# Performance work log

Hardware: AMD Instinct MI355X
Metric: run time of the kernel (lower is better)

The kernel has to match this reference:

```python
import jax, jax.numpy as jnp
import numpy as np

BN_EPS = 1e-5


def cond_conv(x, att_w, att_b, weight, pad):
    """CondConv: per-sample expert-mixed conv.
    x: [N,C,H,W]; att_w: [K,C]; att_b: [K]; weight: [K,O,I,kh,kw]; pad: (ph,pw)."""
    pooled = x.mean(axis=(2, 3))                         # [N,C]  (AdaptiveAvgPool2d(1))
    att = jax.nn.sigmoid(pooled @ att_w.T + att_b)       # [N,K]  (1x1 conv + sigmoid)
    agg_w = jnp.einsum('nk,koihw->noihw', att, weight)   # per-sample kernels [N,O,I,kh,kw]

    def conv1(xi, wi):
        return jax.lax.conv_general_dilated(
            xi[None], wi, window_strides=(1, 1),
            padding=[(pad[0], pad[0]), (pad[1], pad[1])],
            dimension_numbers=('NCHW', 'OIHW', 'NCHW'))[0]

    return jax.vmap(conv1)(x, agg_w)                     # [N,O,H,W]


def batchnorm(x, gamma, beta):
    # training-mode BN: biased batch stats over (N,H,W)
    mean = x.mean(axis=(0, 2, 3), keepdims=True)
    var = x.var(axis=(0, 2, 3), keepdims=True)
    xn = (x - mean) * jax.lax.rsqrt(var + BN_EPS)
    return xn * gamma[None, :, None, None] + beta[None, :, None, None]


def channel_shuffle(x, g):
    N, C, H, W = x.shape
    return x.reshape(N, g, C // g, H, W).transpose(0, 2, 1, 3, 4).reshape(N, C, H, W)


def setup_inputs() -> dict:
    key = jax.random.key(0)
    ks = jax.random.split(key, 8)
    N, C, H, W = 32, 256, 64, 64
    Cb, K = C // 4, 4
    inp = {
        'x': jax.random.normal(ks[0], (N, C, H, W), jnp.float32),
        'sq_att_w': jax.random.normal(ks[1], (K, Cb), jnp.float32) * 0.1,
        'sq_att_b': jnp.zeros((K,), jnp.float32),
        'sq_w': jax.random.normal(ks[2], (K, Cb, Cb, 3, 3), jnp.float32) * 0.05,
        'sq_g': jnp.ones((Cb,), jnp.float32),
        'sq_b': jnp.zeros((Cb,), jnp.float32),
        'ver_att_w': jax.random.normal(ks[3], (K, Cb), jnp.float32) * 0.1,
        'ver_att_b': jnp.zeros((K,), jnp.float32),
        'ver_w': jax.random.normal(ks[4], (K, Cb, Cb, 3, 1), jnp.float32) * 0.05,
        'ver_g': jnp.ones((Cb,), jnp.float32),
        'ver_b': jnp.zeros((Cb,), jnp.float32),
        'hor_att_w': jax.random.normal(ks[5], (K, Cb), jnp.float32) * 0.1,
        'hor_att_b': jnp.zeros((K,), jnp.float32),
        'hor_w': jax.random.normal(ks[6], (K, Cb, Cb, 1, 3), jnp.float32) * 0.05,
        'hor_g': jnp.ones((Cb,), jnp.float32),
        'hor_b': jnp.zeros((Cb,), jnp.float32),
    }
    return inp


def reference(x, sq_att_w, sq_att_b, sq_w, sq_g, sq_b,
              ver_att_w, ver_att_b, ver_w, ver_g, ver_b,
              hor_att_w, hor_att_b, hor_w, hor_g, hor_b):
    # q_Split: chunk into 4 along channels
    s0, s1, s2, s3 = jnp.split(x, 4, axis=1)
    # square branch: CondConv 3x3 pad 1 + BN
    sq = batchnorm(cond_conv(s1, sq_att_w, sq_att_b, sq_w, (1, 1)), sq_g, sq_b)
    # vertical branch: CondConv 3x1 pad (1,0) + BN (crop layer is Identity since offset=0)
    ve = batchnorm(cond_conv(s2, ver_att_w, ver_att_b, ver_w, (1, 0)), ver_g, ver_b)
    # horizontal branch: CondConv 1x3 pad (0,1) + BN
    ho = batchnorm(cond_conv(s3, hor_att_w, hor_att_b, hor_w, (0, 1)), hor_g, hor_b)
    out = jnp.concatenate((s0, sq, ve, ho), axis=1)
    return channel_shuffle(out, 8)
```

## Files before the change

kernel.cpp:

```cpp
#include <hip/hip_runtime.h>
#include <cstddef>
#include <cstdint>


typedef __attribute__((ext_vector_type(8))) short frag8;
typedef __attribute__((ext_vector_type(16))) float accf16;

#define HW 4096
#define CNT_INV (1.0f / 131072.0f)
#define CSTR 1056
#define RSTR 8448
#define XT_BR (32ull * 66 * 8448)

#define WS_POOLED 0
#define WS_SS     6528
#define WS_PST    6912
#define WS_WBF_SQ  203520
#define WS_WBF_VER 793344
#define WS_WBF_HOR 989952
#define WS_XT      1186560
#define WS_CVOUT   14568448

__device__ __forceinline__ int shuf_ch(int c) { return ((c & 31) << 3) | (c >> 5); }

__device__ __forceinline__ unsigned bf16pair(float a, float b) {
    unsigned ua = __builtin_bit_cast(unsigned, a);
    unsigned ub = __builtin_bit_cast(unsigned, b);
    ua = (ua + 0x7fffu + ((ua >> 16) & 1u)) >> 16;
    ub = (ub + 0x7fffu + ((ub >> 16) & 1u)) >> 16;
    return ua | (ub << 16);
}

__device__ __forceinline__ unsigned short bf16r(float a) {
    unsigned ua = __builtin_bit_cast(unsigned, a);
    return (unsigned short)((ua + 0x7fffu + ((ua >> 16) & 1u)) >> 16);
}

__device__ __forceinline__ float bf16lo(unsigned u) {
    return __builtin_bit_cast(float, u << 16);
}
__device__ __forceinline__ float bf16hi(unsigned u) {
    return __builtin_bit_cast(float, u & 0xffff0000u);
}

__device__ __forceinline__ void gload_lds16(const void* g, void* l) {
    __builtin_amdgcn_global_load_lds(
        (const __attribute__((address_space(1))) void*)g,
        (__attribute__((address_space(3))) void*)l, 16, 0, 0);
}

__global__ void __launch_bounds__(256) prepass_kernel(
    const float* __restrict__ x, unsigned char* __restrict__ xt,
    float* __restrict__ pooled, float* __restrict__ out) {
    const int bid = blockIdx.x;
    const int tid = threadIdx.x;

    if (bid >= 768) {
        const int sid = bid - 768;
        const int c8 = sid & 7, n = sid >> 3;
#pragma unroll
        for (int j = 0; j < 8; ++j) {
            const int c = c8 * 8 + j;
            const float4* s = (const float4*)(x + (size_t)(n * 256 + c) * HW);
            float4* d = (float4*)(out + (size_t)(n * 256 + shuf_ch(c)) * HW);
#pragma unroll
            for (int it = 0; it < 4; ++it) d[tid + it * 256] = s[tid + it * 256];
        }
        return;
    }

    const int c8 = bid & 7;
    const int n = (bid >> 3) & 31;
    const int b = bid >> 8;
    const int w = tid & 63, q = tid >> 6;
    const float* xb = x + (size_t)(n * 256 + 64 * (b + 1) + c8 * 8) * HW;
    unsigned char* xtb = xt + (size_t)b * XT_BR + (size_t)n * 66 * RSTR + c8 * CSTR;

    float ps[8] = {0.f, 0.f, 0.f, 0.f, 0.f, 0.f, 0.f, 0.f};
    for (int h = q; h < 64; h += 4) {
        float v[8];
#pragma unroll
        for (int j = 0; j < 8; ++j) v[j] = xb[(size_t)j * HW + h * 64 + w];
        unsigned pk[4];
#pragma unroll
        for (int j = 0; j < 4; ++j) pk[j] = bf16pair(v[2 * j], v[2 * j + 1]);
        *(uint4*)(xtb + (size_t)(h + 1) * RSTR + (w + 1) * 16) = *(uint4*)pk;
#pragma unroll
        for (int j = 0; j < 8; ++j) ps[j] += v[j];
    }
    for (int idx = tid; idx < 260; idx += 256) {
        int p, slot;
        if (idx < 66)       { p = 0;         slot = idx; }
        else if (idx < 132) { p = 65;        slot = idx - 66; }
        else if (idx < 196) { p = idx - 131; slot = 0; }
        else                { p = idx - 195; slot = 65; }
        *(uint4*)(xtb + (size_t)p * RSTR + slot * 16) = uint4{0, 0, 0, 0};
    }
    __shared__ float red[4][8];
#pragma unroll
    for (int j = 0; j < 8; ++j)
#pragma unroll
        for (int off = 32; off; off >>= 1) ps[j] += __shfl_down(ps[j], off, 64);
    if ((tid & 63) == 0)
#pragma unroll
        for (int j = 0; j < 8; ++j) red[q][j] = ps[j];
    __syncthreads();
    if (tid < 8)
        pooled[(b * 32 + n) * 64 + c8 * 8 + tid] =
            (red[0][tid] + red[1][tid] + red[2][tid] + red[3][tid]) * (1.f / 4096.f);
}

template <int TAPS>
__device__ __forceinline__ void aggbf_body(const float* __restrict__ w,
                                           const float* __restrict__ pooled_b,
                                           const float* __restrict__ aw,
                                           const float* __restrict__ ab,
                                           unsigned* __restrict__ wbf, int bid) {
    const int tid = threadIdx.x;
    int idx = bid * 256 + tid;
    int ip = idx & 31;
    int o  = (idx >> 5) & 63;
    int t  = (idx >> 11) % TAPS;
    int n  = (idx >> 11) / TAPS;

    __shared__ float satt[4];
    if (tid < 64) {
        float p = pooled_b[n * 64 + tid];
#pragma unroll
        for (int k = 0; k < 4; ++k) {
            float v = p * aw[k * 64 + tid];
#pragma unroll
            for (int off = 32; off; off >>= 1) v += __shfl_down(v, off, 64);
            if (tid == 0) satt[k] = 1.f / (1.f + expf(-(v + ab[k])));
        }
    }
    __syncthreads();
    const float a0 = satt[0], a1 = satt[1], a2 = satt[2], a3 = satt[3];

    constexpr int PS = 64 * 64 * TAPS;
    int base = (o * 64 + ip * 2) * TAPS + t;
    float v0 = a0*w[base] + a1*w[PS+base] + a2*w[2*PS+base] + a3*w[3*PS+base];
    int base1 = base + TAPS;
    float v1 = a0*w[base1] + a1*w[PS+base1] + a2*w[2*PS+base1] + a3*w[3*PS+base1];
    int f = ip >> 2, jj = ip & 3;
    wbf[(((n * TAPS + t) * 8 + f) * 64 + o) * 4 + jj] = bf16pair(v0, v1);
}

__global__ void __launch_bounds__(256) aggbf_all_kernel(
    const float* __restrict__ pooled,
    const float* __restrict__ aw0, const float* __restrict__ ab0,
    const float* __restrict__ aw1, const float* __restrict__ ab1,
    const float* __restrict__ aw2, const float* __restrict__ ab2,
    const float* __restrict__ sq_w, const float* __restrict__ ver_w,
    const float* __restrict__ hor_w,
    unsigned* __restrict__ wsq, unsigned* __restrict__ wver,
    unsigned* __restrict__ whor) {
    int bid = blockIdx.x;
    if (bid < 2304)
        aggbf_body<9>(sq_w, pooled, aw0, ab0, wsq, bid);
    else if (bid < 3072)
        aggbf_body<3>(ver_w, pooled + 2048, aw1, ab1, wver, bid - 2304);
    else
        aggbf_body<3>(hor_w, pooled + 4096, aw2, ab2, whor, bid - 3072);
}

#define LOADA(dst, tt) \
    _Pragma("unroll") for (int kk = 0; kk < 4; ++kk) { \
        dst[kk]     = wp[(tt) * 512 + kk * 128]; \
        dst[4 + kk] = wp[(tt) * 512 + kk * 128 + 32]; \
    }

#define TAPSTEP(tt, CUR) { \
    const int r_ = (tt) / KW, dw_ = (tt) % KW - PW; \
    const unsigned char* bp_ = xs + (rh * 2 + r_) * RSTR + hi * CSTR + \
                               (wcol + dw_ + 1) * 16; \
    _Pragma("unroll") for (int kk = 0; kk < 4; ++kk) { \
        frag8 b0 = *(const frag8*)(bp_ + kk * 2 * CSTR); \
        frag8 b1 = *(const frag8*)(bp_ + kk * 2 * CSTR + RSTR); \
        a00 = __builtin_amdgcn_mfma_f32_32x32x16_bf16(CUR[kk],     b0, a00, 0, 0, 0); \
        a10 = __builtin_amdgcn_mfma_f32_32x32x16_bf16(CUR[4 + kk], b0, a10, 0, 0, 0); \
        a01 = __builtin_amdgcn_mfma_f32_32x32x16_bf16(CUR[kk],     b1, a01, 0, 0, 0); \
        a11 = __builtin_amdgcn_mfma_f32_32x32x16_bf16(CUR[4 + kk], b1, a11, 0, 0, 0); \
    } }

template <int KH, int KW, int PH, int PW>
__device__ __forceinline__ void conv_body(
    const unsigned char* __restrict__ xt, const unsigned* __restrict__ wbf,
    unsigned short* __restrict__ cvout, float* __restrict__ pst, int cbase,
    int bid, unsigned char* xs, float (*red1)[2][2][16],
    float (*red2)[2][2][16]) {
    constexpr int TAPS = KH * KW;
    constexpr int HB = 4;
    constexpr int ROWS = HB + KH - 1;
    constexpr int TOT = ROWS * RSTR;
    constexpr int NCH = (TOT + 1023) >> 10;
    const int hb = bid & 15, n = bid >> 4;
    const int h0 = hb * HB;
    const int tid = threadIdx.x;
    const int lane = tid & 63;
    const int wv = tid >> 6;
    const int rh = wv >> 1, wn = wv & 1;
    const int l31 = lane & 31, hi = lane >> 5;
    const int wcol = wn * 32 + l31;

    {
        const unsigned char* src = xt +
            (size_t)(n * 66 + h0 + (KH == 1 ? 1 : 0)) * RSTR + lane * 16;
#pragma unroll
        for (int c = wv; c < NCH; c += 4)
            gload_lds16(src + (c << 10), xs + (c << 10));
    }

    const frag8* wp = (const frag8*)wbf + (size_t)n * TAPS * 512 + hi * 64 + l31;

    frag8 aA[8], aB[8];
    LOADA(aA, 0);
    __syncthreads();

    accf16 a00 = {}, a01 = {}, a10 = {}, a11 = {};
#pragma unroll
    for (int t = 0; t < TAPS; t += 2) {
        if (t + 1 < TAPS) LOADA(aB, t + 1);
        TAPSTEP(t, aA);
        if (t + 2 < TAPS) LOADA(aA, t + 2);
        if (t + 1 < TAPS) TAPSTEP(t + 1, aB);
    }

    {
        unsigned short* cb = cvout + (size_t)(n * 192 + (cbase - 64)) * HW +
                             (h0 + rh * 2) * 64 + wcol;
#pragma unroll
        for (int rg = 0; rg < 16; ++rg) {
            const int o = (rg & 3) + 8 * (rg >> 2) + 4 * hi;
            unsigned short* p0 = cb + (size_t)o * HW;
            p0[0]  = bf16r(a00[rg]);
            p0[64] = bf16r(a01[rg]);
            unsigned short* p1 = cb + (size_t)(o + 32) * HW;
            p1[0]  = bf16r(a10[rg]);
            p1[64] = bf16r(a11[rg]);
        }
    }

#pragma unroll
    for (int rg = 0; rg < 16; ++rg) {
        float u1 = a00[rg] + a01[rg];
        float u2 = a00[rg] * a00[rg] + a01[rg] * a01[rg];
        float w1 = a10[rg] + a11[rg];
        float w2 = a10[rg] * a10[rg] + a11[rg] * a11[rg];
#pragma unroll
        for (int off = 16; off; off >>= 1) {
            u1 += __shfl_down(u1, off, 32);
            u2 += __shfl_down(u2, off, 32);
            w1 += __shfl_down(w1, off, 32);
            w2 += __shfl_down(w2, off, 32);
        }
        if (l31 == 0) {
            red1[wv][0][hi][rg] = u1; red2[wv][0][hi][rg] = u2;
            red1[wv][1][hi][rg] = w1; red2[wv][1][hi][rg] = w2;
        }
    }
    __syncthreads();
    if (tid < 64) {
        const int rg = tid & 15, hi2 = (tid >> 4) & 1, wm2 = tid >> 5;
        float s1 = 0.f, s2 = 0.f;
#pragma unroll
        for (int v = 0; v < 4; ++v) {
            s1 += red1[v][wm2][hi2][rg];
            s2 += red2[v][wm2][hi2][rg];
        }
        const int o = wm2 * 32 + (rg & 3) + 8 * (rg >> 2) + 4 * hi2;
        const int slot = n * 16 + hb;
        pst[o * 1024 + slot] = s1;
        pst[o * 1024 + 512 + slot] = s2;
    }
}

__global__ void __launch_bounds__(256, 3) conv_all_kernel(
    const unsigned char* __restrict__ xt,
    const unsigned* __restrict__ wsq, const unsigned* __restrict__ wver,
    const unsigned* __restrict__ whor,
    unsigned short* __restrict__ cvout, float* __restrict__ pst) {
    __shared__ __align__(16) unsigned char xs[6 * RSTR + 512];
    __shared__ float red1[4][2][2][16], red2[4][2][2][16];
    int bid = (blockIdx.x & 7) * 192 + (blockIdx.x >> 3);
    if (bid < 512)
        conv_body<3, 3, 1, 1>(xt, wsq, cvout, pst, 64, bid, xs, red1, red2);
    else if (bid < 1024)
        conv_body<3, 1, 1, 0>(xt + XT_BR, wver, cvout, pst + 65536, 128,
                              bid - 512, xs, red1, red2);
    else
        conv_body<1, 3, 0, 1>(xt + 2 * XT_BR, whor, cvout, pst + 131072, 192,
                              bid - 1024, xs, red1, red2);
}

__global__ void __launch_bounds__(256) bnstats_all_kernel(
    const float* __restrict__ pst,
    const float* __restrict__ g0, const float* __restrict__ b0,
    const float* __restrict__ g1, const float* __restrict__ b1,
    const float* __restrict__ g2, const float* __restrict__ b2,
    float* __restrict__ ss) {
    int br = blockIdx.x >> 6, o = blockIdx.x & 63, t = threadIdx.x;
    const float* gamma = (br == 0) ? g0 : (br == 1) ? g1 : g2;
    const float* beta  = (br == 0) ? b0 : (br == 1) ? b1 : b2;
    const float* p = pst + br * 65536 + o * 1024;
    float s1 = 0.f, s2 = 0.f;
    for (int i = t; i < 512; i += 256) {
        s1 += p[i];
        s2 += p[512 + i];
    }
#pragma unroll
    for (int off = 32; off; off >>= 1) {
        s1 += __shfl_down(s1, off, 64);
        s2 += __shfl_down(s2, off, 64);
    }
    __shared__ float r1[4], r2[4];
    if ((t & 63) == 0) { r1[t >> 6] = s1; r2[t >> 6] = s2; }
    __syncthreads();
    if (t == 0) {
        float S1 = r1[0] + r1[1] + r1[2] + r1[3];
        float S2 = r2[0] + r2[1] + r2[2] + r2[3];
        float mean = S1 * CNT_INV;
        float var = S2 * CNT_INV - mean * mean;
        float scale = rsqrtf(var + 1e-5f) * gamma[o];
        ss[br * 128 + o * 2 + 0] = scale;
        ss[br * 128 + o * 2 + 1] = beta[o] - mean * scale;
    }
}

__global__ void __launch_bounds__(256) bn_all_kernel(
    const unsigned short* __restrict__ cvout, float* __restrict__ out,
    const float* __restrict__ ss) {
    int g = blockIdx.x;
    int half = g & 1;
    int n = (g >> 1) & 31;
    int o = (g >> 6) & 63;
    int sub = g >> 12;
    float scale = ss[sub * 128 + o * 2], shift = ss[sub * 128 + o * 2 + 1];
    const uint4* src = (const uint4*)(cvout +
        (size_t)(n * 192 + sub * 64 + o) * HW + half * 2048) + threadIdx.x;
    float* dst = out + (size_t)(n * 256 + shuf_ch(64 * (sub + 1) + o)) * HW +
                 half * 2048 + threadIdx.x * 8;
    uint4 r = *src;
    float4 f0, f1;
    f0.x = fmaf(bf16lo(r.x), scale, shift);
    f0.y = fmaf(bf16hi(r.x), scale, shift);
    f0.z = fmaf(bf16lo(r.y), scale, shift);
    f0.w = fmaf(bf16hi(r.y), scale, shift);
    f1.x = fmaf(bf16lo(r.z), scale, shift);
    f1.y = fmaf(bf16hi(r.z), scale, shift);
    f1.z = fmaf(bf16lo(r.w), scale, shift);
    f1.w = fmaf(bf16hi(r.w), scale, shift);
    *(float4*)dst = f0;
    *(float4*)(dst + 4) = f1;
}

extern "C" void kernel_launch(void* const* d_in, const int* in_sizes, int n_in,
                              void* d_out, int out_size, void* d_ws, size_t ws_size,
                              hipStream_t stream) {
    const float* x        = (const float*)d_in[0];
    const float* sq_att_w = (const float*)d_in[1];
    const float* sq_att_b = (const float*)d_in[2];
    const float* sq_w     = (const float*)d_in[3];
    const float* sq_g     = (const float*)d_in[4];
    const float* sq_b     = (const float*)d_in[5];
    const float* ver_att_w= (const float*)d_in[6];
    const float* ver_att_b= (const float*)d_in[7];
    const float* ver_w    = (const float*)d_in[8];
    const float* ver_g    = (const float*)d_in[9];
    const float* ver_b    = (const float*)d_in[10];
    const float* hor_att_w= (const float*)d_in[11];
    const float* hor_att_b= (const float*)d_in[12];
    const float* hor_w    = (const float*)d_in[13];
    const float* hor_g    = (const float*)d_in[14];
    const float* hor_b    = (const float*)d_in[15];
    float* out = (float*)d_out;
    float* ws = (float*)d_ws;

    float* pooled = ws + WS_POOLED;
    float* ss     = ws + WS_SS;
    float* pst    = ws + WS_PST;
    unsigned* wbf_sq  = (unsigned*)(ws + WS_WBF_SQ);
    unsigned* wbf_ver = (unsigned*)(ws + WS_WBF_VER);
    unsigned* wbf_hor = (unsigned*)(ws + WS_WBF_HOR);
    unsigned char* xt = (unsigned char*)(ws + WS_XT);
    unsigned short* cvout = (unsigned short*)(ws + WS_CVOUT);

    prepass_kernel<<<1024, 256, 0, stream>>>(x, xt, pooled, out);
    aggbf_all_kernel<<<3840, 256, 0, stream>>>(pooled,
                                               sq_att_w, sq_att_b,
                                               ver_att_w, ver_att_b,
                                               hor_att_w, hor_att_b,
                                               sq_w, ver_w, hor_w,
                                               wbf_sq, wbf_ver, wbf_hor);
    conv_all_kernel<<<1536, 256, 0, stream>>>(xt, wbf_sq, wbf_ver, wbf_hor,
                                              cvout, pst);
    bnstats_all_kernel<<<192, 256, 0, stream>>>(pst, sq_g, sq_b, ver_g, ver_b,
                                                hor_g, hor_b, ss);
    bn_all_kernel<<<12288, 256, 0, stream>>>(cvout, out, ss);
}
```

Measured before the change: 161.7 us.

## Split prepass over height quarters and move s0 copy into conv kernel

The prepass kernel is split four ways along height, tripling its block count, and writes partial pooled sums per quarter. The aggregation kernel now sums those four partials itself. The passthrough copy of the untouched channel group moves from the prepass into extra blocks at the tail of the conv kernel, so it can overlap with compute-bound conv work. Workspace offsets shift to make room for the larger pooled buffer. The risks are small extra reads in the aggregation kernel and possible memory contention between the copy blocks and the conv blocks.

```diff
diff --git a/kernel.cpp b/kernel.cpp
--- a/kernel.cpp
+++ b/kernel.cpp
@@ -13,13 +13,13 @@
 #define XT_BR (32ull * 66 * 8448)
 
 #define WS_POOLED 0
-#define WS_SS     6528
-#define WS_PST    6912
-#define WS_WBF_SQ  203520
-#define WS_WBF_VER 793344
-#define WS_WBF_HOR 989952
-#define WS_XT      1186560
-#define WS_CVOUT   14568448
+#define WS_SS     24576
+#define WS_PST    24960
+#define WS_WBF_SQ  221568
+#define WS_WBF_VER 811392
+#define WS_WBF_HOR 1008000
+#define WS_XT      1204608
+#define WS_CVOUT   14586240
 
 __device__ __forceinline__ int shuf_ch(int c) { return ((c & 31) << 3) | (c >> 5); }
 
@@ -51,33 +51,21 @@
 
 __global__ void __launch_bounds__(256) prepass_kernel(
     const float* __restrict__ x, unsigned char* __restrict__ xt,
-    float* __restrict__ pooled, float* __restrict__ out) {
+    float* __restrict__ pooled4) {
     const int bid = blockIdx.x;
+    const int hq = bid & 3;
+    const int c8 = (bid >> 2) & 7;
+    const int n = (bid >> 5) & 31;
+    const int b = bid >> 10;
     const int tid = threadIdx.x;
-
-    if (bid >= 768) {
-        const int sid = bid - 768;
-        const int c8 = sid & 7, n = sid >> 3;
-#pragma unroll
-        for (int j = 0; j < 8; ++j) {
-            const int c = c8 * 8 + j;
-            const float4* s = (const float4*)(x + (size_t)(n * 256 + c) * HW);
-            float4* d = (float4*)(out + (size_t)(n * 256 + shuf_ch(c)) * HW);
-#pragma unroll
-            for (int it = 0; it < 4; ++it) d[tid + it * 256] = s[tid + it * 256];
-        }
-        return;
-    }
-
-    const int c8 = bid & 7;
-    const int n = (bid >> 3) & 31;
-    const int b = bid >> 8;
     const int w = tid & 63, q = tid >> 6;
     const float* xb = x + (size_t)(n * 256 + 64 * (b + 1) + c8 * 8) * HW;
     unsigned char* xtb = xt + (size_t)b * XT_BR + (size_t)n * 66 * RSTR + c8 * CSTR;
 
     float ps[8] = {0.f, 0.f, 0.f, 0.f, 0.f, 0.f, 0.f, 0.f};
-    for (int h = q; h < 64; h += 4) {
+#pragma unroll
+    for (int it = 0; it < 4; ++it) {
+        const int h = hq * 16 + it * 4 + q;
         float v[8];
 #pragma unroll
         for (int j = 0; j < 8; ++j) v[j] = xb[(size_t)j * HW + h * 64 + w];
@@ -88,13 +76,15 @@
 #pragma unroll
         for (int j = 0; j < 8; ++j) ps[j] += v[j];
     }
-    for (int idx = tid; idx < 260; idx += 256) {
-        int p, slot;
-        if (idx < 66)       { p = 0;         slot = idx; }
-        else if (idx < 132) { p = 65;        slot = idx - 66; }
-        else if (idx < 196) { p = idx - 131; slot = 0; }
-        else                { p = idx - 195; slot = 65; }
-        *(uint4*)(xtb + (size_t)p * RSTR + slot * 16) = uint4{0, 0, 0, 0};
+    if (hq == 0) {
+        for (int idx = tid; idx < 260; idx += 256) {
+            int p, slot;
+            if (idx < 66)       { p = 0;         slot = idx; }
+            else if (idx < 132) { p = 65;        slot = idx - 66; }
+            else if (idx < 196) { p = idx - 131; slot = 0; }
+            else                { p = idx - 195; slot = 65; }
+            *(uint4*)(xtb + (size_t)p * RSTR + slot * 16) = uint4{0, 0, 0, 0};
+        }
     }
     __shared__ float red[4][8];
 #pragma unroll
@@ -106,8 +96,8 @@
         for (int j = 0; j < 8; ++j) red[q][j] = ps[j];
     __syncthreads();
     if (tid < 8)
-        pooled[(b * 32 + n) * 64 + c8 * 8 + tid] =
-            (red[0][tid] + red[1][tid] + red[2][tid] + red[3][tid]) * (1.f / 4096.f);
+        pooled4[hq * 6144 + (b * 32 + n) * 64 + c8 * 8 + tid] =
+            red[0][tid] + red[1][tid] + red[2][tid] + red[3][tid];
 }
 
 template <int TAPS>
@@ -125,7 +115,10 @@
 
     __shared__ float satt[4];
     if (tid < 64) {
-        float p = pooled_b[n * 64 + tid];
+        const int base = n * 64 + tid;
+        float p = (pooled_b[base] + pooled_b[base + 6144] +
+                   pooled_b[base + 12288] + pooled_b[base + 18432]) *
+                  (1.f / 4096.f);
 #pragma unroll
         for (int k = 0; k < 4; ++k) {
             float v = p * aw[k * 64 + tid];
@@ -275,14 +268,30 @@
     }
 }
 
+__device__ __forceinline__ void s0_body(const float* __restrict__ x,
+                                        float* __restrict__ out, int sid) {
+    const int c8 = sid & 7, n = sid >> 3, tid = threadIdx.x;
+#pragma unroll
+    for (int j = 0; j < 8; ++j) {
+        const int c = c8 * 8 + j;
+        const float4* s = (const float4*)(x + (size_t)(n * 256 + c) * HW);
+        float4* d = (float4*)(out + (size_t)(n * 256 + shuf_ch(c)) * HW);
+#pragma unroll
+        for (int it = 0; it < 4; ++it) d[tid + it * 256] = s[tid + it * 256];
+    }
+}
+
 __global__ void __launch_bounds__(256, 3) conv_all_kernel(
-    const unsigned char* __restrict__ xt,
+    const float* __restrict__ x, const unsigned char* __restrict__ xt,
     const unsigned* __restrict__ wsq, const unsigned* __restrict__ wver,
     const unsigned* __restrict__ whor,
-    unsigned short* __restrict__ cvout, float* __restrict__ pst) {
+    unsigned short* __restrict__ cvout, float* __restrict__ pst,
+    float* __restrict__ out) {
     __shared__ __align__(16) unsigned char xs[6 * RSTR + 512];
     __shared__ float red1[4][2][2][16], red2[4][2][2][16];
-    int bid = (blockIdx.x & 7) * 192 + (blockIdx.x >> 3);
+    int raw = blockIdx.x;
+    if (raw >= 1536) { s0_body(x, out, raw - 1536); return; }
+    int bid = (raw & 7) * 192 + (raw >> 3);
     if (bid < 512)
         conv_body<3, 3, 1, 1>(xt, wsq, cvout, pst, 64, bid, xs, red1, red2);
     else if (bid < 1024)
@@ -385,15 +394,15 @@
     unsigned char* xt = (unsigned char*)(ws + WS_XT);
     unsigned short* cvout = (unsigned short*)(ws + WS_CVOUT);
 
-    prepass_kernel<<<1024, 256, 0, stream>>>(x, xt, pooled, out);
+    prepass_kernel<<<3072, 256, 0, stream>>>(x, xt, pooled);
     aggbf_all_kernel<<<3840, 256, 0, stream>>>(pooled,
                                                sq_att_w, sq_att_b,
                                                ver_att_w, ver_att_b,
                                                hor_att_w, hor_att_b,
                                                sq_w, ver_w, hor_w,
                                                wbf_sq, wbf_ver, wbf_hor);
-    conv_all_kernel<<<1536, 256, 0, stream>>>(xt, wbf_sq, wbf_ver, wbf_hor,
-                                              cvout, pst);
+    conv_all_kernel<<<1792, 256, 0, stream>>>(x, xt, wbf_sq, wbf_ver, wbf_hor,
+                                              cvout, pst, out);
     bnstats_all_kernel<<<192, 256, 0, stream>>>(pst, sq_g, sq_b, ver_g, ver_b,
                                                 hor_g, hor_b, ss);
     bn_all_kernel<<<12288, 256, 0, stream>>>(cvout, out, ss);
```

New measurement: 144.0 us. -11.0%, faster.
